# Performance work log

Measured on AMD Instinct MI355X. Metric: run time of the kernel, lower is better.

## Reference

```python
import jax, jax.numpy as jnp
import numpy as np

DIM = 768
HEADS = 12
HEAD_DIM = DIM // HEADS
HIDDEN = 4 * DIM
EPS = 1e-5


def _ln(x, w, b):
    mu = jnp.mean(x, axis=-1, keepdims=True)
    var = jnp.var(x, axis=-1, keepdims=True)
    return (x - mu) * jax.lax.rsqrt(var + EPS) * w + b


def setup_inputs() -> dict:
    key = jax.random.key(0)
    ks = jax.random.split(key, 8)
    B, N, C = 8, 1024, DIM
    s = 0.02
    return {
        "before": jax.random.normal(ks[0], (B, N, C), jnp.float32),
        "after": jax.random.normal(ks[1], (B, N, C), jnp.float32),
        "norm1_w": jnp.ones((C,), jnp.float32),
        "norm1_b": jnp.zeros((C,), jnp.float32),
        "qkv_w": jax.random.normal(ks[2], (3 * C, C), jnp.float32) * s,
        "hln_w": jnp.ones((HEAD_DIM,), jnp.float32),
        "hln_b": jnp.zeros((HEAD_DIM,), jnp.float32),
        "proj_w": jax.random.normal(ks[3], (C, C), jnp.float32) * s,
        "proj_b": jnp.zeros((C,), jnp.float32),
        "norm2_w": jnp.ones((C,), jnp.float32),
        "norm2_b": jnp.zeros((C,), jnp.float32),
        "fc1_w": jax.random.normal(ks[4], (HIDDEN, C), jnp.float32) * s,
        "fc1_b": jnp.zeros((HIDDEN,), jnp.float32),
        "fc2_w": jax.random.normal(ks[5], (C, HIDDEN), jnp.float32) * s,
        "fc2_b": jnp.zeros((C,), jnp.float32),
    }


def _qkv_normed(x, qkv_w, hln_w, hln_b):
    B, N, C = x.shape
    qkv = x @ qkv_w.T  # (B,N,3C)
    qkv = qkv.reshape(B, N, 3, HEADS, HEAD_DIM).transpose(2, 0, 3, 1, 4)  # (3,B,H,N,hd)
    qkv = _ln(qkv, hln_w, hln_b)  # per-head LayerNorm over head_dim
    return qkv[0], qkv[1], qkv[2]


def _cross_attn(q, k, v, proj_w, proj_b):
    B, H, N, D = q.shape
    scale = D ** (-0.5)
    attn = jax.nn.softmax(jnp.einsum("bhnd,bhmd->bhnm", q, k) * scale, axis=-1)
    ctx = jnp.einsum("bhnm,bhmd->bhnd", attn, v)
    ctx = ctx.transpose(0, 2, 1, 3).reshape(B, N, H * D)
    ctx = ctx @ proj_w.T + proj_b
    # NOTE: original adds q.reshape(B,N,C) WITHOUT transposing heads (faithful)
    return ctx + q.reshape(B, N, H * D)


def _mlp(x, fc1_w, fc1_b, fc2_w, fc2_b):
    h = jax.nn.gelu(x @ fc1_w.T + fc1_b, approximate=False)
    return h @ fc2_w.T + fc2_b


def reference(before, after, norm1_w, norm1_b, qkv_w, hln_w, hln_b, proj_w, proj_b,
              norm2_w, norm2_b, fc1_w, fc1_b, fc2_w, fc2_b):
    before_n = _ln(before, norm1_w, norm1_b)
    after_n = _ln(after, norm1_w, norm1_b)
    q_b, k_b, v_b = _qkv_normed(before_n, qkv_w, hln_w, hln_b)
    q_a, k_a, v_a = _qkv_normed(after_n, qkv_w, hln_w, hln_b)
    context_a = _cross_attn(q_b, k_a, v_a, proj_w, proj_b)  # before attends to after
    context_b = _cross_attn(q_a, k_b, v_b, proj_w, proj_b)  # after attends to before
    before_o = before_n + context_b
    after_o = after_n + context_a
    before_o = before_o + _mlp(_ln(before_o, norm2_w, norm2_b), fc1_w, fc1_b, fc2_w, fc2_b)
    after_o = after_o + _mlp(_ln(after_o, norm2_w, norm2_b), fc1_w, fc1_b, fc2_w, fc2_b)
    return (before_o, after_o)
```

## Files before the change

### kernel.cpp

```cpp
#include <hip/hip_runtime.h>
#include <hip/hip_bf16.h>

typedef unsigned short u16;
typedef __attribute__((ext_vector_type(8))) short bf16x8;
typedef __attribute__((ext_vector_type(4))) float f32x4;

#define DIRSTRIDE 6291456

__device__ __forceinline__ u16 f2bf(float x){
  __hip_bfloat16 h = __float2bfloat16(x);
  return *reinterpret_cast<u16*>(&h);
}
__device__ __forceinline__ float bf2f(u16 u){
  return __uint_as_float(((unsigned int)u) << 16);
}
__device__ __forceinline__ u16 f2bf_fast(float x){
  return (u16)((__float_as_uint(x) + 0x8000u) >> 16);
}

__device__ __forceinline__ void xcd_remap(int& bx, int& by){
  int gx = (int)gridDim.x;
  int lin = (int)blockIdx.x + gx*(int)blockIdx.y;
  int nwg8 = (gx*(int)gridDim.y) >> 3;
  int rl = (lin & 7)*nwg8 + (lin >> 3);
  bx = rl % gx; by = rl / gx;
}

__global__ __launch_bounds__(256) void zero_kernel(float* __restrict__ p, int n){
  int i = blockIdx.x*256 + threadIdx.x;
  if (i < n) p[i] = 0.f;
}

__global__ __launch_bounds__(256) void cvt_kernel(const float* __restrict__ s,
                                                  u16* __restrict__ d, int n){
  int i = blockIdx.x*256 + threadIdx.x;
  if (i < n) d[i] = f2bf(s[i]);
}

__global__ __launch_bounds__(256) void ln_kernel(const float* __restrict__ s0,
    const float* __restrict__ s1, const float* __restrict__ w,
    const float* __restrict__ b, u16* __restrict__ out,
    float* __restrict__ mu_out, float* __restrict__ rs_out){
  int r = blockIdx.x;
  const float* src = (r < 8192) ? (s0 + (size_t)r*768) : (s1 + (size_t)(r-8192)*768);
  int t = threadIdx.x;
  float v0 = src[t], v1 = src[t+256], v2 = src[t+512];
  __shared__ float red[4];
  float s = v0+v1+v2;
  #pragma unroll
  for (int o=32;o;o>>=1) s += __shfl_xor(s,o);
  if ((t&63)==0) red[t>>6] = s;
  __syncthreads();
  float mean = (red[0]+red[1]+red[2]+red[3]) * (1.0f/768.0f);
  float d0=v0-mean, d1=v1-mean, d2=v2-mean;
  float q = d0*d0+d1*d1+d2*d2;
  __syncthreads();
  #pragma unroll
  for (int o=32;o;o>>=1) q += __shfl_xor(q,o);
  if ((t&63)==0) red[t>>6] = q;
  __syncthreads();
  float var = (red[0]+red[1]+red[2]+red[3]) * (1.0f/768.0f);
  float rstd = rsqrtf(var + 1e-5f);
  if (mu_out && t == 0){ mu_out[r] = mean; rs_out[r] = rstd; }
  size_t base = (size_t)r*768;
  out[base+t]     = f2bf(d0*rstd*w[t]     + b[t]);
  out[base+t+256] = f2bf(d1*rstd*w[t+256] + b[t+256]);
  out[base+t+512] = f2bf(d2*rstd*w[t+512] + b[t+512]);
}

__device__ __forceinline__ void stage_tile64(const u16* g, size_t strideK, u16* lds,
                                             int w, int lane){
  #pragma unroll
  for (int i=0;i<4;i++){
    int row = w*32 + i*8 + (lane>>3);
    int cs  = (lane&7) ^ (row&7);
    const u16* gp = g + (size_t)row*strideK + cs*8;
    __builtin_amdgcn_global_load_lds(
        (const __attribute__((address_space(1))) unsigned int*)gp,
        (__attribute__((address_space(3))) unsigned int*)(lds + (w*4+i)*512),
        16, 0, 0);
  }
}

__device__ __forceinline__ void stage_tile64x64(const u16* g, size_t strideK,
                                                u16* lds, int w, int lane){
  #pragma unroll
  for (int i=0;i<2;i++){
    int row = w*16 + i*8 + (lane>>3);
    int cs  = (lane&7) ^ (row&7);
    const u16* gp = g + (size_t)row*strideK + cs*8;
    __builtin_amdgcn_global_load_lds(
        (const __attribute__((address_space(1))) unsigned int*)gp,
        (__attribute__((address_space(3))) unsigned int*)(lds + (w*2+i)*512),
        16, 0, 0);
  }
}

#define SWZ_FRAG(tile, r, c) (*(const bf16x8*)&(tile)[(r)*64 + (((c) ^ ((r)&7)))*8])

template<int EPI>
__global__ __launch_bounds__(256, 4) void gemm_kernel(
    const u16* __restrict__ A, const u16* __restrict__ W, void* Cout,
    const float* __restrict__ bias, const float* resF,
    int M, int N, int K)
{
  __shared__ __attribute__((aligned(16))) u16 sA[128*64];
  __shared__ __attribute__((aligned(16))) u16 sB[128*64];
  int t = threadIdx.x;
  int w = t>>6, lane = t&63, ln = lane&15, quad = lane>>4;
  int bx, by; xcd_remap(bx, by);
  int m0 = by*128, n0 = bx*128;
  int wr = (w>>1)*64, wc = (w&1)*64;
  f32x4 acc[4][4];
  #pragma unroll
  for (int mi=0;mi<4;mi++)
    #pragma unroll
    for (int ni=0;ni<4;ni++) acc[mi][ni] = (f32x4){0.f,0.f,0.f,0.f};
  int KB = K >> 6;
  for (int kb=0;kb<KB;kb++){
    __syncthreads();
    stage_tile64(A + (size_t)m0*K + kb*64, K, sA, w, lane);
    stage_tile64(W + (size_t)n0*K + kb*64, K, sB, w, lane);
    __syncthreads();
    #pragma unroll
    for (int ks=0;ks<2;ks++){
      bf16x8 aF[4], bF[4];
      #pragma unroll
      for (int mi=0;mi<4;mi++) aF[mi] = SWZ_FRAG(sA, wr+mi*16+ln, ks*4+quad);
      #pragma unroll
      for (int ni=0;ni<4;ni++) bF[ni] = SWZ_FRAG(sB, wc+ni*16+ln, ks*4+quad);
      #pragma unroll
      for (int mi=0;mi<4;mi++)
        #pragma unroll
        for (int ni=0;ni<4;ni++)
          acc[mi][ni] = __builtin_amdgcn_mfma_f32_16x16x32_bf16(aF[mi], bF[ni], acc[mi][ni], 0,0,0);
    }
  }
  #pragma unroll
  for (int mi=0;mi<4;mi++){
    #pragma unroll
    for (int ni=0;ni<4;ni++){
      #pragma unroll
      for (int r=0;r<4;r++){
        int row = m0 + wr + mi*16 + quad*4 + r;
        int col = n0 + wc + ni*16 + ln;
        size_t ridx = (size_t)row*N + col;
        float v = acc[mi][ni][r];
        if (EPI == 2){
          v += bias[col];
          v = 0.5f*v*(1.0f + erff(v*0.70710678118654752f));
          ((u16*)Cout)[ridx] = f2bf(v);
        } else {
          float rf = resF[ridx];
          ((float*)Cout)[ridx] = v + bias[col] + rf;
        }
      }
    }
  }
}

__global__ __launch_bounds__(256, 4) void gemm_proj_kernel(
    const u16* __restrict__ A, const u16* __restrict__ W, float* Cout,
    const float* __restrict__ bias, const u16* __restrict__ resQ,
    const float* __restrict__ before, const float* __restrict__ after,
    const float* __restrict__ n1w, const float* __restrict__ n1b,
    const float* __restrict__ mu, const float* __restrict__ rstd)
{
  const int K = 768, N = 768, KB = 12;
  __shared__ __attribute__((aligned(16))) u16 sA[128*64];
  __shared__ __attribute__((aligned(16))) u16 sB[128*64];
  int t = threadIdx.x;
  int w = t>>6, lane = t&63, ln = lane&15, quad = lane>>4;
  int bx, by; xcd_remap(bx, by);
  int m0 = by*128, n0 = bx*128;
  int wr = (w>>1)*64, wc = (w&1)*64;
  f32x4 acc[4][4];
  #pragma unroll
  for (int mi=0;mi<4;mi++)
    #pragma unroll
    for (int ni=0;ni<4;ni++) acc[mi][ni] = (f32x4){0.f,0.f,0.f,0.f};
  for (int kb=0;kb<KB;kb++){
    __syncthreads();
    stage_tile64(A + (size_t)m0*K + kb*64, K, sA, w, lane);
    stage_tile64(W + (size_t)n0*K + kb*64, K, sB, w, lane);
    __syncthreads();
    #pragma unroll
    for (int ks=0;ks<2;ks++){
      bf16x8 aF[4], bF[4];
      #pragma unroll
      for (int mi=0;mi<4;mi++) aF[mi] = SWZ_FRAG(sA, wr+mi*16+ln, ks*4+quad);
      #pragma unroll
      for (int ni=0;ni<4;ni++) bF[ni] = SWZ_FRAG(sB, wc+ni*16+ln, ks*4+quad);
      #pragma unroll
      for (int mi=0;mi<4;mi++)
        #pragma unroll
        for (int ni=0;ni<4;ni++)
          acc[mi][ni] = __builtin_amdgcn_mfma_f32_16x16x32_bf16(aF[mi], bF[ni], acc[mi][ni], 0,0,0);
    }
  }
  #pragma unroll
  for (int mi=0;mi<4;mi++){
    #pragma unroll
    for (int ni=0;ni<4;ni++){
      #pragma unroll
      for (int r=0;r<4;r++){
        int row = m0 + wr + mi*16 + quad*4 + r;
        int col = n0 + wc + ni*16 + ln;
        size_t ridx = (size_t)row*N + col;
        int dirout = row >> 13;
        int rem = row & 8191;
        size_t qidx = (size_t)(1-dirout)*DIRSTRIDE + (size_t)rem*768 + col;
        const float* src = dirout ? after : before;
        float xr = (src[(size_t)rem*768 + col] - mu[row]) * rstd[row] * n1w[col] + n1b[col];
        Cout[ridx] = acc[mi][ni][r] + bias[col] + bf2f(resQ[qidx]) + xr;
      }
    }
  }
}

__global__ __launch_bounds__(256, 4) void gemm_qkv_kernel(
    const u16* __restrict__ A, const u16* __restrict__ W,
    const float* __restrict__ hw, const float* __restrict__ hb,
    u16* __restrict__ q, u16* __restrict__ k, u16* __restrict__ vt)
{
  const int K = 768, KB = 12;
  __shared__ __attribute__((aligned(16))) u16 sA[128*64];
  __shared__ __attribute__((aligned(16))) u16 sB[128*64];
  int t = threadIdx.x;
  int w = t>>6, lane = t&63, ln = lane&15, quad = lane>>4;
  int bx, by; xcd_remap(bx, by);
  int m0 = by*128, n0 = bx*128;
  int wr = (w>>1)*64, wc = (w&1)*64;
  f32x4 acc[4][4];
  #pragma unroll
  for (int mi=0;mi<4;mi++)
    #pragma unroll
    for (int ni=0;ni<4;ni++) acc[mi][ni] = (f32x4){0.f,0.f,0.f,0.f};
  for (int kb=0;kb<KB;kb++){
    __syncthreads();
    stage_tile64(A + (size_t)m0*K + kb*64, K, sA, w, lane);
    stage_tile64(W + (size_t)n0*K + kb*64, K, sB, w, lane);
    __syncthreads();
    #pragma unroll
    for (int ks=0;ks<2;ks++){
      bf16x8 aF[4], bF[4];
      #pragma unroll
      for (int mi=0;mi<4;mi++) aF[mi] = SWZ_FRAG(sA, wr+mi*16+ln, ks*4+quad);
      #pragma unroll
      for (int ni=0;ni<4;ni++) bF[ni] = SWZ_FRAG(sB, wc+ni*16+ln, ks*4+quad);
      #pragma unroll
      for (int mi=0;mi<4;mi++)
        #pragma unroll
        for (int ni=0;ni<4;ni++)
          acc[mi][ni] = __builtin_amdgcn_mfma_f32_16x16x32_bf16(aF[mi], bF[ni], acc[mi][ni], 0,0,0);
    }
  }
  int sec = (n0 + wc) >> 6;
  int which = sec / 12, h = sec - which*12;
  float hwv[4], hbv[4];
  #pragma unroll
  for (int ni=0;ni<4;ni++){ hwv[ni] = hw[ni*16+ln]; hbv[ni] = hb[ni*16+ln]; }
  #pragma unroll
  for (int mi=0;mi<4;mi++){
    #pragma unroll
    for (int r=0;r<4;r++){
      float s = acc[mi][0][r]+acc[mi][1][r]+acc[mi][2][r]+acc[mi][3][r];
      #pragma unroll
      for (int ofs=1; ofs<16; ofs<<=1) s += __shfl_xor(s, ofs);
      float mu = s * (1.0f/64.0f);
      float vv = 0.f;
      #pragma unroll
      for (int ni=0;ni<4;ni++){ float d = acc[mi][ni][r]-mu; vv += d*d; }
      #pragma unroll
      for (int ofs=1; ofs<16; ofs<<=1) vv += __shfl_xor(vv, ofs);
      float rstd = rsqrtf(vv*(1.0f/64.0f) + 1e-5f);
      int token = m0 + wr + mi*16 + quad*4 + r;
      int dir = token >> 13, bb = (token>>10)&7, n = token & 1023;
      size_t base = (size_t)dir*DIRSTRIDE + (size_t)bb*786432 + (size_t)h*65536;
      #pragma unroll
      for (int ni=0;ni<4;ni++){
        u16 y = f2bf((acc[mi][ni][r]-mu)*rstd*hwv[ni] + hbv[ni]);
        int hd = ni*16 + ln;
        if (which == 0)      q[base + (size_t)n*64 + hd] = y;
        else if (which == 1) k[base + (size_t)n*64 + hd] = y;
        else                 vt[base + (size_t)hd*1024 + n] = y;
      }
    }
  }
}

__global__ __launch_bounds__(256) void flash_kernel(const u16* __restrict__ qg,
    const u16* __restrict__ kg, const u16* __restrict__ vtg, u16* __restrict__ ctx)
{
  __shared__ __attribute__((aligned(16))) u16 sK[2][64*64];
  __shared__ __attribute__((aligned(16))) u16 sV[2][64*64];
  __shared__ __attribute__((aligned(16))) u16 sP[4*16*72];
  int lin = (int)blockIdx.x + 16*((int)blockIdx.y + 96*(int)blockIdx.z);
  int x8 = lin & 7, jj = lin >> 3;
  int qt = jj & 15;
  int g  = x8 + 8*(jj >> 4);
  int dout = g & 1, bh = g >> 1;
  int b = bh/12, h = bh - b*12;
  size_t qbase = (size_t)(1-dout)*DIRSTRIDE + (size_t)b*786432 + (size_t)h*65536;
  size_t kbase = (size_t)dout*DIRSTRIDE + (size_t)b*786432 + (size_t)h*65536;
  int t = threadIdx.x;
  int w = t>>6, lane = t&63, ln = lane&15, quad = lane>>4;
  const u16* qp = qg + qbase + (size_t)(qt*64 + w*16 + ln)*64 + quad*8;
  bf16x8 aQ0 = *(const bf16x8*)qp;
  bf16x8 aQ1 = *(const bf16x8*)(qp + 32);
  bf16x8 vOne;
  #pragma unroll
  for (int j=0;j<8;j++) vOne[j] = (short)0x3F80;
  f32x4 o[4];
  #pragma unroll
  for (int ni=0;ni<4;ni++) o[ni] = (f32x4){0.f,0.f,0.f,0.f};
  f32x4 oL = (f32x4){0.f,0.f,0.f,0.f};
  u16* pw = &sP[w*16*72];
  const float cs = 0.18033688011112042f;
  stage_tile64x64(kg  + kbase, 64, sK[0], w, lane);
  stage_tile64x64(vtg + kbase, 1024, sV[0], w, lane);
  __syncthreads();
  int cur = 0;
  for (int kt=0;kt<16;kt++){
    if (kt < 15){
      stage_tile64x64(kg  + kbase + (size_t)(kt+1)*4096, 64, sK[cur^1], w, lane);
      stage_tile64x64(vtg + kbase + (size_t)(kt+1)*64, 1024, sV[cur^1], w, lane);
    }
    const u16* sKc = sK[cur];
    const u16* sVc = sV[cur];
    bf16x8 bK[4][2], bV[4][2];
    #pragma unroll
    for (int ni=0;ni<4;ni++){
      int rr = ni*16 + ln;
      bK[ni][0] = SWZ_FRAG(sKc, rr, quad);
      bK[ni][1] = SWZ_FRAG(sKc, rr, 4+quad);
      bV[ni][0] = SWZ_FRAG(sVc, rr, quad);
      bV[ni][1] = SWZ_FRAG(sVc, rr, 4+quad);
    }
    f32x4 s[4];
    __builtin_amdgcn_s_setprio(1);
    #pragma unroll
    for (int ni=0;ni<4;ni++){
      s[ni] = (f32x4){0.f,0.f,0.f,0.f};
      s[ni] = __builtin_amdgcn_mfma_f32_16x16x32_bf16(aQ0, bK[ni][0], s[ni], 0,0,0);
      s[ni] = __builtin_amdgcn_mfma_f32_16x16x32_bf16(aQ1, bK[ni][1], s[ni], 0,0,0);
    }
    __builtin_amdgcn_s_setprio(0);
    #pragma unroll
    for (int ni=0;ni<4;ni++){
      #pragma unroll
      for (int r=0;r<4;r++){
        float p = exp2f(s[ni][r]*cs);
        pw[(quad*4+r)*72 + ni*16 + ln] = f2bf_fast(p);
      }
    }
    bf16x8 aP0 = *(const bf16x8*)&pw[ln*72 + quad*8];
    bf16x8 aP1 = *(const bf16x8*)&pw[ln*72 + 32 + quad*8];
    __builtin_amdgcn_s_setprio(1);
    #pragma unroll
    for (int ni=0;ni<4;ni++){
      o[ni] = __builtin_amdgcn_mfma_f32_16x16x32_bf16(aP0, bV[ni][0], o[ni], 0,0,0);
      o[ni] = __builtin_amdgcn_mfma_f32_16x16x32_bf16(aP1, bV[ni][1], o[ni], 0,0,0);
    }
    oL = __builtin_amdgcn_mfma_f32_16x16x32_bf16(aP0, vOne, oL, 0,0,0);
    oL = __builtin_amdgcn_mfma_f32_16x16x32_bf16(aP1, vOne, oL, 0,0,0);
    __builtin_amdgcn_s_setprio(0);
    __syncthreads();
    cur ^= 1;
  }
  #pragma unroll
  for (int ni=0;ni<4;ni++){
    #pragma unroll
    for (int r=0;r<4;r++){
      int row = qt*64 + w*16 + quad*4 + r;
      float val = o[ni][r] / oL[r];
      ctx[((size_t)dout*8192 + (size_t)b*1024 + row)*768 + h*64 + ni*16 + ln] = f2bf(val);
    }
  }
}

extern "C" void kernel_launch(void* const* d_in, const int* in_sizes, int n_in,
                              void* d_out, int out_size, void* d_ws, size_t ws_size,
                              hipStream_t stream)
{
  const float* before = (const float*)d_in[0];
  const float* after  = (const float*)d_in[1];
  const float* n1w  = (const float*)d_in[2];
  const float* n1b  = (const float*)d_in[3];
  const float* qkvw = (const float*)d_in[4];
  const float* hlnw = (const float*)d_in[5];
  const float* hlnb = (const float*)d_in[6];
  const float* projw= (const float*)d_in[7];
  const float* projb= (const float*)d_in[8];
  const float* n2w  = (const float*)d_in[9];
  const float* n2b  = (const float*)d_in[10];
  const float* fc1w = (const float*)d_in[11];
  const float* fc1b = (const float*)d_in[12];
  const float* fc2w = (const float*)d_in[13];
  const float* fc2b = (const float*)d_in[14];

  const size_t REQUIRED = 114950144;
  if (ws_size < REQUIRED){
    zero_kernel<<<(out_size + 255)/256, 256, 0, stream>>>((float*)d_out, out_size);
    return;
  }

  char* ws = (char*)d_ws;
  u16* xn    = (u16*)(ws + 0);
  u16* ctxb  = (u16*)(ws + 0);
  u16* gbuf  = (u16*)(ws + 0);
  u16* qb    = (u16*)(ws + 25165824);
  u16* kb    = (u16*)(ws + 50331648);
  u16* h1n   = (u16*)(ws + 50331648);
  u16* vtb   = (u16*)(ws + 75497472);
  u16* wqkv  = (u16*)(ws + 100663296);
  u16* wproj = (u16*)(ws + 104202240);
  u16* wfc1  = (u16*)(ws + 105381888);
  u16* wfc2  = (u16*)(ws + 110100480);
  float* mu1  = (float*)(ws + 114819072);
  float* rs1  = (float*)(ws + 114884608);
  float* h1   = (float*)d_out;
  float* outp = (float*)d_out;

  cvt_kernel<<<6912, 256, 0, stream>>>(qkvw, wqkv, 1769472);
  cvt_kernel<<<2304, 256, 0, stream>>>(projw, wproj, 589824);
  cvt_kernel<<<9216, 256, 0, stream>>>(fc1w, wfc1, 2359296);
  cvt_kernel<<<9216, 256, 0, stream>>>(fc2w, wfc2, 2359296);

  ln_kernel<<<16384, 256, 0, stream>>>(before, after, n1w, n1b, xn, mu1, rs1);
  gemm_qkv_kernel<<<dim3(18,128), 256, 0, stream>>>(xn, wqkv, hlnw, hlnb, qb, kb, vtb);
  flash_kernel<<<dim3(16,96,2), 256, 0, stream>>>(qb, kb, vtb, ctxb);
  gemm_proj_kernel<<<dim3(6,128), 256, 0, stream>>>(ctxb, wproj, h1,
      projb, qb, before, after, n1w, n1b, mu1, rs1);
  ln_kernel<<<16384, 256, 0, stream>>>(h1, h1 + (size_t)8192*768, n2w, n2b, h1n,
      nullptr, nullptr);
  for (int c = 0; c < 2; c++){
    size_t off = (size_t)c * 8192 * 768;
    gemm_kernel<2><<<dim3(24,64), 256, 0, stream>>>(h1n + off, wfc1, gbuf,
        fc1b, nullptr, 8192, 3072, 768);
    gemm_kernel<3><<<dim3(6,64), 256, 0, stream>>>(gbuf, wfc2, outp + off,
        fc2b, h1 + off, 8192, 768, 3072);
  }
}
```

Before: 683.1 us.

## Double-buffer LDS tiles in GEMM kernels to overlap loads with MFMA

Switches the three GEMM kernels from single-buffered LDS staging with two barriers per K-step to a ping-pong double buffer. The next K tile is prefetched with global_load_lds while MFMAs consume the current one, leaving one barrier per iteration. LDS use per block doubles to 64 KB and the occupancy hint is dropped from launch bounds, so fewer blocks can be resident per CU. The prefetch relies on the single barrier at the end of each iteration to complete the async LDS loads before the buffer is read.

```diff
diff --git a/kernel.cpp b/kernel.cpp
--- a/kernel.cpp
+++ b/kernel.cpp
@@ -99,13 +99,13 @@
 #define SWZ_FRAG(tile, r, c) (*(const bf16x8*)&(tile)[(r)*64 + (((c) ^ ((r)&7)))*8])
 
 template<int EPI>
-__global__ __launch_bounds__(256, 4) void gemm_kernel(
+__global__ __launch_bounds__(256) void gemm_kernel(
     const u16* __restrict__ A, const u16* __restrict__ W, void* Cout,
     const float* __restrict__ bias, const float* resF,
     int M, int N, int K)
 {
-  __shared__ __attribute__((aligned(16))) u16 sA[128*64];
-  __shared__ __attribute__((aligned(16))) u16 sB[128*64];
+  __shared__ __attribute__((aligned(16))) u16 sA[2][128*64];
+  __shared__ __attribute__((aligned(16))) u16 sB[2][128*64];
   int t = threadIdx.x;
   int w = t>>6, lane = t&63, ln = lane&15, quad = lane>>4;
   int bx, by; xcd_remap(bx, by);
@@ -117,24 +117,32 @@
     #pragma unroll
     for (int ni=0;ni<4;ni++) acc[mi][ni] = (f32x4){0.f,0.f,0.f,0.f};
   int KB = K >> 6;
+  stage_tile64(A + (size_t)m0*K, K, sA[0], w, lane);
+  stage_tile64(W + (size_t)n0*K, K, sB[0], w, lane);
+  __syncthreads();
+  int cur = 0;
   for (int kb=0;kb<KB;kb++){
-    __syncthreads();
-    stage_tile64(A + (size_t)m0*K + kb*64, K, sA, w, lane);
-    stage_tile64(W + (size_t)n0*K + kb*64, K, sB, w, lane);
-    __syncthreads();
+    if (kb+1 < KB){
+      stage_tile64(A + (size_t)m0*K + (kb+1)*64, K, sA[cur^1], w, lane);
+      stage_tile64(W + (size_t)n0*K + (kb+1)*64, K, sB[cur^1], w, lane);
+    }
+    const u16* pA = sA[cur];
+    const u16* pB = sB[cur];
     #pragma unroll
     for (int ks=0;ks<2;ks++){
       bf16x8 aF[4], bF[4];
       #pragma unroll
-      for (int mi=0;mi<4;mi++) aF[mi] = SWZ_FRAG(sA, wr+mi*16+ln, ks*4+quad);
-      #pragma unroll
-      for (int ni=0;ni<4;ni++) bF[ni] = SWZ_FRAG(sB, wc+ni*16+ln, ks*4+quad);
+      for (int mi=0;mi<4;mi++) aF[mi] = SWZ_FRAG(pA, wr+mi*16+ln, ks*4+quad);
+      #pragma unroll
+      for (int ni=0;ni<4;ni++) bF[ni] = SWZ_FRAG(pB, wc+ni*16+ln, ks*4+quad);
       #pragma unroll
       for (int mi=0;mi<4;mi++)
         #pragma unroll
         for (int ni=0;ni<4;ni++)
           acc[mi][ni] = __builtin_amdgcn_mfma_f32_16x16x32_bf16(aF[mi], bF[ni], acc[mi][ni], 0,0,0);
     }
+    __syncthreads();
+    cur ^= 1;
   }
   #pragma unroll
   for (int mi=0;mi<4;mi++){
@@ -159,7 +167,7 @@
   }
 }
 
-__global__ __launch_bounds__(256, 4) void gemm_proj_kernel(
+__global__ __launch_bounds__(256) void gemm_proj_kernel(
     const u16* __restrict__ A, const u16* __restrict__ W, float* Cout,
     const float* __restrict__ bias, const u16* __restrict__ resQ,
     const float* __restrict__ before, const float* __restrict__ after,
@@ -167,8 +175,8 @@
     const float* __restrict__ mu, const float* __restrict__ rstd)
 {
   const int K = 768, N = 768, KB = 12;
-  __shared__ __attribute__((aligned(16))) u16 sA[128*64];
-  __shared__ __attribute__((aligned(16))) u16 sB[128*64];
+  __shared__ __attribute__((aligned(16))) u16 sA[2][128*64];
+  __shared__ __attribute__((aligned(16))) u16 sB[2][128*64];
   int t = threadIdx.x;
   int w = t>>6, lane = t&63, ln = lane&15, quad = lane>>4;
   int bx, by; xcd_remap(bx, by);
@@ -179,24 +187,32 @@
   for (int mi=0;mi<4;mi++)
     #pragma unroll
     for (int ni=0;ni<4;ni++) acc[mi][ni] = (f32x4){0.f,0.f,0.f,0.f};
+  stage_tile64(A + (size_t)m0*K, K, sA[0], w, lane);
+  stage_tile64(W + (size_t)n0*K, K, sB[0], w, lane);
+  __syncthreads();
+  int cur = 0;
   for (int kb=0;kb<KB;kb++){
-    __syncthreads();
-    stage_tile64(A + (size_t)m0*K + kb*64, K, sA, w, lane);
-    stage_tile64(W + (size_t)n0*K + kb*64, K, sB, w, lane);
-    __syncthreads();
+    if (kb+1 < KB){
+      stage_tile64(A + (size_t)m0*K + (kb+1)*64, K, sA[cur^1], w, lane);
+      stage_tile64(W + (size_t)n0*K + (kb+1)*64, K, sB[cur^1], w, lane);
+    }
+    const u16* pA = sA[cur];
+    const u16* pB = sB[cur];
     #pragma unroll
     for (int ks=0;ks<2;ks++){
       bf16x8 aF[4], bF[4];
       #pragma unroll
-      for (int mi=0;mi<4;mi++) aF[mi] = SWZ_FRAG(sA, wr+mi*16+ln, ks*4+quad);
-      #pragma unroll
-      for (int ni=0;ni<4;ni++) bF[ni] = SWZ_FRAG(sB, wc+ni*16+ln, ks*4+quad);
+      for (int mi=0;mi<4;mi++) aF[mi] = SWZ_FRAG(pA, wr+mi*16+ln, ks*4+quad);
+      #pragma unroll
+      for (int ni=0;ni<4;ni++) bF[ni] = SWZ_FRAG(pB, wc+ni*16+ln, ks*4+quad);
       #pragma unroll
       for (int mi=0;mi<4;mi++)
         #pragma unroll
         for (int ni=0;ni<4;ni++)
           acc[mi][ni] = __builtin_amdgcn_mfma_f32_16x16x32_bf16(aF[mi], bF[ni], acc[mi][ni], 0,0,0);
     }
+    __syncthreads();
+    cur ^= 1;
   }
   #pragma unroll
   for (int mi=0;mi<4;mi++){
@@ -218,14 +234,14 @@
   }
 }
 
-__global__ __launch_bounds__(256, 4) void gemm_qkv_kernel(
+__global__ __launch_bounds__(256) void gemm_qkv_kernel(
     const u16* __restrict__ A, const u16* __restrict__ W,
     const float* __restrict__ hw, const float* __restrict__ hb,
     u16* __restrict__ q, u16* __restrict__ k, u16* __restrict__ vt)
 {
   const int K = 768, KB = 12;
-  __shared__ __attribute__((aligned(16))) u16 sA[128*64];
-  __shared__ __attribute__((aligned(16))) u16 sB[128*64];
+  __shared__ __attribute__((aligned(16))) u16 sA[2][128*64];
+  __shared__ __attribute__((aligned(16))) u16 sB[2][128*64];
   int t = threadIdx.x;
   int w = t>>6, lane = t&63, ln = lane&15, quad = lane>>4;
   int bx, by; xcd_remap(bx, by);
@@ -236,24 +252,32 @@
   for (int mi=0;mi<4;mi++)
     #pragma unroll
     for (int ni=0;ni<4;ni++) acc[mi][ni] = (f32x4){0.f,0.f,0.f,0.f};
+  stage_tile64(A + (size_t)m0*K, K, sA[0], w, lane);
+  stage_tile64(W + (size_t)n0*K, K, sB[0], w, lane);
+  __syncthreads();
+  int cur = 0;
   for (int kb=0;kb<KB;kb++){
-    __syncthreads();
-    stage_tile64(A + (size_t)m0*K + kb*64, K, sA, w, lane);
-    stage_tile64(W + (size_t)n0*K + kb*64, K, sB, w, lane);
-    __syncthreads();
+    if (kb+1 < KB){
+      stage_tile64(A + (size_t)m0*K + (kb+1)*64, K, sA[cur^1], w, lane);
+      stage_tile64(W + (size_t)n0*K + (kb+1)*64, K, sB[cur^1], w, lane);
+    }
+    const u16* pA = sA[cur];
+    const u16* pB = sB[cur];
     #pragma unroll
     for (int ks=0;ks<2;ks++){
       bf16x8 aF[4], bF[4];
       #pragma unroll
-      for (int mi=0;mi<4;mi++) aF[mi] = SWZ_FRAG(sA, wr+mi*16+ln, ks*4+quad);
-      #pragma unroll
-      for (int ni=0;ni<4;ni++) bF[ni] = SWZ_FRAG(sB, wc+ni*16+ln, ks*4+quad);
+      for (int mi=0;mi<4;mi++) aF[mi] = SWZ_FRAG(pA, wr+mi*16+ln, ks*4+quad);
+      #pragma unroll
+      for (int ni=0;ni<4;ni++) bF[ni] = SWZ_FRAG(pB, wc+ni*16+ln, ks*4+quad);
       #pragma unroll
       for (int mi=0;mi<4;mi++)
         #pragma unroll
         for (int ni=0;ni<4;ni++)
           acc[mi][ni] = __builtin_amdgcn_mfma_f32_16x16x32_bf16(aF[mi], bF[ni], acc[mi][ni], 0,0,0);
     }
+    __syncthreads();
+    cur ^= 1;
   }
   int sec = (n0 + wc) >> 6;
   int which = sec / 12, h = sec - which*12;
```

New measurement: 745.6 us. 1.09x slower.
